# Optimization experiments

Hardware: AMD Instinct MI355X
Metric: run time of the kernel (lower is better)

The kernel has to match this reference:

```python
import jax, jax.numpy as jnp
import numpy as np

B, S, H, D = 4, 2048, 8, 64  # batch, seq, heads, per-head dim (dim=64)
EPS = 1e-5


def _layernorm(h, g, b):
    m = jnp.mean(h, axis=-1, keepdims=True)
    v = jnp.mean(jnp.square(h - m), axis=-1, keepdims=True)
    return (h - m) * jax.lax.rsqrt(v + EPS) * g + b


def setup_inputs() -> dict:
    key = jax.random.key(0)
    ks = jax.random.split(key, 12)
    s = 1.0 / np.sqrt(D)
    return {
        "x": jax.random.normal(ks[0], (B, S, H, D), dtype=jnp.float32),
        "ln1_g": jnp.ones((D,), jnp.float32),
        "ln1_b": jnp.zeros((D,), jnp.float32),
        "Wp": jax.random.normal(ks[1], (D, 3 * D), jnp.float32) * s,
        "bp": jnp.zeros((3 * D,), jnp.float32),
        "ln2_g": jnp.ones((D,), jnp.float32),
        "ln2_b": jnp.zeros((D,), jnp.float32),
        "W1": jax.random.normal(ks[2], (D, 4 * D), jnp.float32) * s,
        "b1": jnp.zeros((4 * D,), jnp.float32),
        "W2": jax.random.normal(ks[3], (4 * D, D), jnp.float32) * (1.0 / np.sqrt(4 * D)),
        "b2": jnp.zeros((D,), jnp.float32),
    }


def reference(x, ln1_g, ln1_b, Wp, bp, ln2_g, ln2_b, W1, b1, W2, b2):
    # x: [B, S, H, D]
    h = _layernorm(x, ln1_g, ln1_b)
    qkv = h @ Wp + bp                       # [B,S,H,3D]  (dropout = identity, eval)
    q, k, v = jnp.split(qkv, 3, axis=-1)
    q = q.transpose(0, 2, 1, 3)             # [B,H,S,D]
    k = k.transpose(0, 2, 1, 3)
    v = v.transpose(0, 2, 1, 3)
    sim = jnp.einsum('bhqd,bhkd->bhqk', q, k)   # no sqrt(d) scaling (faithful)
    attn = jax.nn.softmax(sim, axis=-1)
    out = jnp.einsum('bhqk,bhkd->bhqd', attn, v).transpose(0, 2, 1, 3)  # [B,S,H,D]
    out = _layernorm(out, ln2_g, ln2_b)
    out = jax.nn.gelu(out @ W1 + b1, approximate=False) @ W2 + b2
    return out + x
```

## Files before the change

### kernel.cpp

```cpp
#include <hip/hip_runtime.h>
#include <hip/hip_bf16.h>
#include <math.h>

#define BB 4
#define SS 2048
#define HH 8
#define DD 64
#define EPSV 1e-5f

typedef __attribute__((ext_vector_type(8))) short short8;
typedef __attribute__((ext_vector_type(4))) float f32x4;
typedef __attribute__((ext_vector_type(4))) unsigned int uint4v;
typedef unsigned short ushort_t;
#define MFMA16 __builtin_amdgcn_mfma_f32_16x16x32_bf16

__device__ inline unsigned short f2bf(float f) {
    unsigned u = __builtin_bit_cast(unsigned, f);
    unsigned r = (u + 0x7fffu + ((u >> 16) & 1u)) >> 16;
    return (unsigned short)r;
}
__device__ inline float bf2f(unsigned short h) {
    unsigned u = ((unsigned)h) << 16;
    return __builtin_bit_cast(float, u);
}
__device__ inline unsigned pkbf(float a, float b) {
    __hip_bfloat162 h2 = __float22bfloat162_rn(make_float2(a, b));
    unsigned u;
    __builtin_memcpy(&u, &h2, 4);
    return u;
}

__global__ __launch_bounds__(256) void k0_prep(
    const float* __restrict__ Wp, const float* __restrict__ W1,
    const float* __restrict__ W2, ushort_t* __restrict__ WpTh,
    ushort_t* __restrict__ WpTl, ushort_t* __restrict__ W1T,
    ushort_t* __restrict__ W2T)
{
    int gid = blockIdx.x * 256 + threadIdx.x;
    if (gid < 12288) {
        int n = gid >> 6, k = gid & 63;
        float w = Wp[k * 192 + n];
        ushort_t hi = f2bf(w);
        WpTh[gid] = hi;
        WpTl[gid] = f2bf(w - bf2f(hi));
    }
    {
        int n = gid >> 6, k = gid & 63;
        W1T[gid] = f2bf(W1[k * 256 + n]);
    }
    {
        int n = gid >> 8, k = gid & 255;
        W2T[gid] = f2bf(W2[k * 64 + n]);
    }
}

__global__ __launch_bounds__(256) void k1_ln_qkv(
    const float* __restrict__ x, const float* __restrict__ g1, const float* __restrict__ b1v,
    const ushort_t* __restrict__ WpTh, const ushort_t* __restrict__ WpTl,
    const float* __restrict__ bp,
    float* __restrict__ qws, ushort_t* __restrict__ khws, ushort_t* __restrict__ vtws)
{
    __shared__ __align__(16) ushort_t Hh[64 * 72];
    __shared__ __align__(16) ushort_t Hl[64 * 72];
    __shared__ __align__(16) ushort_t Vt[64 * 72];

    const int tid = threadIdx.x;
    const int wv  = tid >> 6;
    const int lane = tid & 63;
    const int l15 = lane & 15;
    const int g   = lane >> 4;
    const int bh  = blockIdx.x & 31;
    const int sc  = blockIdx.x >> 5;
    const int b   = bh >> 3, hh = bh & 7;
    const int s0  = sc * 64;

    short8 bqh[2], bql[2], bkh[2], bkl[2], bvh[2];
    #pragma unroll
    for (int kh = 0; kh < 2; ++kh) {
        int koff = kh * 32 + g * 8;
        bqh[kh] = *(const short8*)(WpTh + (wv * 16 + l15) * 64 + koff);
        bql[kh] = *(const short8*)(WpTl + (wv * 16 + l15) * 64 + koff);
        bkh[kh] = *(const short8*)(WpTh + (64 + wv * 16 + l15) * 64 + koff);
        bkl[kh] = *(const short8*)(WpTl + (64 + wv * 16 + l15) * 64 + koff);
        bvh[kh] = *(const short8*)(WpTh + (128 + wv * 16 + l15) * 64 + koff);
    }
    const float biasq = bp[wv * 16 + l15];
    const float biask = bp[64 + wv * 16 + l15];
    const float biasv = bp[128 + wv * 16 + l15];

    {
        const int srow = s0 + wv * 16 + l15;
        const float* xr = x + ((size_t)(b * 2048 + srow) * 8 + hh) * 64;
        float hvv[16];
        #pragma unroll
        for (int kh = 0; kh < 2; ++kh) {
            float4 p0 = *(const float4*)(xr + kh * 32 + g * 8);
            float4 p1 = *(const float4*)(xr + kh * 32 + g * 8 + 4);
            hvv[kh*8+0]=p0.x; hvv[kh*8+1]=p0.y; hvv[kh*8+2]=p0.z; hvv[kh*8+3]=p0.w;
            hvv[kh*8+4]=p1.x; hvv[kh*8+5]=p1.y; hvv[kh*8+6]=p1.z; hvv[kh*8+7]=p1.w;
        }
        float s1 = 0.0f;
        #pragma unroll
        for (int i = 0; i < 16; ++i) s1 += hvv[i];
        s1 += __shfl_xor(s1, 16, 64);
        s1 += __shfl_xor(s1, 32, 64);
        float mean = s1 * (1.0f / 64.0f);
        float s2 = 0.0f;
        #pragma unroll
        for (int i = 0; i < 16; ++i) { float d = hvv[i] - mean; s2 += d * d; }
        s2 += __shfl_xor(s2, 16, 64);
        s2 += __shfl_xor(s2, 32, 64);
        float rstd = rsqrtf(s2 * (1.0f / 64.0f) + EPSV);

        #pragma unroll
        for (int kh = 0; kh < 2; ++kh) {
            ushort_t hi[8]; unsigned lo2[4];
            float hf[8];
            #pragma unroll
            for (int j = 0; j < 8; ++j) {
                int dI = kh * 32 + g * 8 + j;
                hf[j] = (hvv[kh*8+j] - mean) * rstd * g1[dI] + b1v[dI];
                hi[j] = f2bf(hf[j]);
            }
            uint4 HHv;
            HHv.x = (unsigned)hi[0] | ((unsigned)hi[1] << 16);
            HHv.y = (unsigned)hi[2] | ((unsigned)hi[3] << 16);
            HHv.z = (unsigned)hi[4] | ((unsigned)hi[5] << 16);
            HHv.w = (unsigned)hi[6] | ((unsigned)hi[7] << 16);
            #pragma unroll
            for (int j = 0; j < 4; ++j)
                lo2[j] = pkbf(hf[2*j] - bf2f(hi[2*j]), hf[2*j+1] - bf2f(hi[2*j+1]));
            uint4 HLv; HLv.x = lo2[0]; HLv.y = lo2[1]; HLv.z = lo2[2]; HLv.w = lo2[3];
            int off = (wv * 16 + l15) * 72 + kh * 32 + g * 8;
            *(uint4*)(&Hh[off]) = HHv;
            *(uint4*)(&Hl[off]) = HLv;
        }
    }
    __syncthreads();

    #pragma unroll
    for (int mt = 0; mt < 4; ++mt) {
        short8 ah[2], al[2];
        int abase = (mt * 16 + l15) * 72 + g * 8;
        ah[0] = *(const short8*)(&Hh[abase]);
        ah[1] = *(const short8*)(&Hh[abase + 32]);
        al[0] = *(const short8*)(&Hl[abase]);
        al[1] = *(const short8*)(&Hl[abase + 32]);

        f32x4 aq = (f32x4){0.f,0.f,0.f,0.f};
        f32x4 ak = (f32x4){0.f,0.f,0.f,0.f};
        f32x4 av = (f32x4){0.f,0.f,0.f,0.f};
        #pragma unroll
        for (int kh = 0; kh < 2; ++kh) {
            aq = MFMA16(ah[kh], bqh[kh], aq, 0, 0, 0);
            aq = MFMA16(al[kh], bqh[kh], aq, 0, 0, 0);
            aq = MFMA16(ah[kh], bql[kh], aq, 0, 0, 0);
            ak = MFMA16(ah[kh], bkh[kh], ak, 0, 0, 0);
            ak = MFMA16(al[kh], bkh[kh], ak, 0, 0, 0);
            ak = MFMA16(ah[kh], bkl[kh], ak, 0, 0, 0);
            av = MFMA16(ah[kh], bvh[kh], av, 0, 0, 0);
        }

        size_t base = ((size_t)bh * 2048 + s0 + mt * 16 + 4 * g) * 64 + wv * 16 + l15;
        #pragma unroll
        for (int r = 0; r < 4; ++r) {
            qws[base + (size_t)r * 64] = aq[r] + biasq;
            khws[base + (size_t)r * 64] = f2bf(ak[r] + biask);
        }
        uint2 vvp;
        vvp.x = pkbf(av[0] + biasv, av[1] + biasv);
        vvp.y = pkbf(av[2] + biasv, av[3] + biasv);
        *(uint2*)(&Vt[(wv * 16 + l15) * 72 + mt * 16 + 4 * g]) = vvp;
    }
    __syncthreads();

    #pragma unroll
    for (int p = 0; p < 2; ++p) {
        int slot = tid + 256 * p;
        int dd = slot >> 3, cc = slot & 7;
        int c0 = ((cc >> 2) << 5) + ((cc & 3) << 2);
        uint2 a = *(const uint2*)(&Vt[dd * 72 + c0]);
        uint2 b2 = *(const uint2*)(&Vt[dd * 72 + c0 + 16]);
        uint4 o; o.x = a.x; o.y = a.y; o.z = b2.x; o.w = b2.y;
        *(uint4*)(vtws + ((size_t)bh * 64 + dd) * 2048 + s0 + cc * 8) = o;
    }
}

#define LROW 72
#define NKT 32

__global__ __launch_bounds__(256, 4) void k2_attn(
    const float* __restrict__ qws, const ushort_t* __restrict__ khws,
    const ushort_t* __restrict__ vtws, float* __restrict__ ows)
{
    __shared__ __align__(16) ushort_t KhL[2][64 * LROW];
    __shared__ __align__(16) ushort_t VtL[2][64 * LROW];

    const int tid  = threadIdx.x;
    const int w    = tid >> 6;
    const int lane = tid & 63;
    const int l15  = lane & 15;
    const int g    = lane >> 4;
    const int bh   = blockIdx.x & 31;
    const int qb0  = (blockIdx.x >> 5) * 128;

    const float LOG2E = 1.4426950408889634f;
    short8 qh[2][2], ql[2][2];
    #pragma unroll
    for (int sub = 0; sub < 2; ++sub) {
        const float* qp = qws + ((size_t)bh * SS + qb0 + w * 32 + sub * 16 + l15) * 64;
        #pragma unroll
        for (int kh = 0; kh < 2; ++kh) {
            const float* p = qp + 32 * kh + 8 * g;
            #pragma unroll
            for (int j = 0; j < 8; ++j) {
                float f = p[j] * LOG2E;
                ushort_t hi = f2bf(f);
                qh[sub][kh][j] = (short)hi;
                ql[sub][kh][j] = (short)f2bf(f - bf2f(hi));
            }
        }
    }

    float lrow[2] = {0.0f, 0.0f};
    f32x4 oacc[2][4];
    #pragma unroll
    for (int sub = 0; sub < 2; ++sub)
        #pragma unroll
        for (int dt = 0; dt < 4; ++dt) oacc[sub][dt] = (f32x4){0.f, 0.f, 0.f, 0.f};

    const size_t kbase = (size_t)bh * SS * 64;
    const size_t vbase = (size_t)bh * 64 * 2048;

    uint4 kb[2], vb[2];
    #pragma unroll
    for (int rr = 0; rr < 2; ++rr) {
        int slot = tid + 256 * rr;
        int row = slot >> 3, seg = slot & 7;
        kb[rr] = *(const uint4*)(khws + kbase + (size_t)row * 64 + seg * 8);
        vb[rr] = *(const uint4*)(vtws + vbase + (size_t)row * 2048 + seg * 8);
    }
    #pragma unroll
    for (int rr = 0; rr < 2; ++rr) {
        int slot = tid + 256 * rr;
        int row = slot >> 3, seg = slot & 7;
        *(uint4*)(&KhL[0][row * LROW + seg * 8]) = kb[rr];
        *(uint4*)(&VtL[0][row * LROW + seg * 8]) = vb[rr];
    }

    for (int kt = 0; kt < NKT; ++kt) {
        __syncthreads();
        const int cur = kt & 1;

        if (kt < NKT - 1) {
            #pragma unroll
            for (int rr = 0; rr < 2; ++rr) {
                int slot = tid + 256 * rr;
                int row = slot >> 3, seg = slot & 7;
                kb[rr] = *(const uint4*)(khws + kbase + (size_t)((kt + 1) * 64 + row) * 64 + seg * 8);
                vb[rr] = *(const uint4*)(vtws + vbase + (size_t)row * 2048 + (kt + 1) * 64 + seg * 8);
            }
        }

        #pragma unroll
        for (int half = 0; half < 2; ++half) {
            uint2 pA[2], pB[2];
            #pragma unroll
            for (int nf2 = 0; nf2 < 2; ++nf2) {
                const int nf = half * 2 + nf2;
                f32x4 aA = (f32x4){0.f, 0.f, 0.f, 0.f};
                f32x4 aB = (f32x4){0.f, 0.f, 0.f, 0.f};
                #pragma unroll
                for (int kh = 0; kh < 2; ++kh) {
                    short8 kah = *(const short8*)(&KhL[cur][(nf * 16 + l15) * LROW + 32 * kh + 8 * g]);
                    aA = MFMA16(kah, qh[0][kh], aA, 0, 0, 0);
                    aA = MFMA16(kah, ql[0][kh], aA, 0, 0, 0);
                    aB = MFMA16(kah, qh[1][kh], aB, 0, 0, 0);
                    aB = MFMA16(kah, ql[1][kh], aB, 0, 0, 0);
                }
                {
                    float p0 = __builtin_amdgcn_exp2f(aA[0]);
                    float p1 = __builtin_amdgcn_exp2f(aA[1]);
                    float p2 = __builtin_amdgcn_exp2f(aA[2]);
                    float p3 = __builtin_amdgcn_exp2f(aA[3]);
                    lrow[0] += (p0 + p1) + (p2 + p3);
                    pA[nf2].x = pkbf(p0, p1); pA[nf2].y = pkbf(p2, p3);
                }
                {
                    float p0 = __builtin_amdgcn_exp2f(aB[0]);
                    float p1 = __builtin_amdgcn_exp2f(aB[1]);
                    float p2 = __builtin_amdgcn_exp2f(aB[2]);
                    float p3 = __builtin_amdgcn_exp2f(aB[3]);
                    lrow[1] += (p0 + p1) + (p2 + p3);
                    pB[nf2].x = pkbf(p0, p1); pB[nf2].y = pkbf(p2, p3);
                }
            }
            short8 paA = __builtin_bit_cast(short8, (uint4v){pA[0].x, pA[0].y, pA[1].x, pA[1].y});
            short8 paB = __builtin_bit_cast(short8, (uint4v){pB[0].x, pB[0].y, pB[1].x, pB[1].y});
            #pragma unroll
            for (int dt = 0; dt < 4; ++dt) {
                short8 vbf = *(const short8*)(&VtL[cur][(16 * dt + l15) * LROW + half * 32 + 8 * g]);
                oacc[0][dt] = MFMA16(paA, vbf, oacc[0][dt], 0, 0, 0);
                oacc[1][dt] = MFMA16(paB, vbf, oacc[1][dt], 0, 0, 0);
            }
        }

        if (kt < NKT - 1) {
            #pragma unroll
            for (int rr = 0; rr < 2; ++rr) {
                int slot = tid + 256 * rr;
                int row = slot >> 3, seg = slot & 7;
                *(uint4*)(&KhL[cur ^ 1][row * LROW + seg * 8]) = kb[rr];
                *(uint4*)(&VtL[cur ^ 1][row * LROW + seg * 8]) = vb[rr];
            }
        }
    }

    #pragma unroll
    for (int sub = 0; sub < 2; ++sub) {
        float l = lrow[sub];
        l += __shfl_xor(l, 16, 64);
        l += __shfl_xor(l, 32, 64);
        float il = 1.0f / l;
        #pragma unroll
        for (int r = 0; r < 4; ++r) {
            float ilr = __shfl(il, 4 * g + r, 64);
            int row = qb0 + w * 32 + sub * 16 + 4 * g + r;
            #pragma unroll
            for (int dt = 0; dt < 4; ++dt)
                ows[((size_t)bh * SS + row) * 64 + dt * 16 + l15] = oacc[sub][dt][r] * ilr;
        }
    }
}

#define ITERS 4

__global__ __launch_bounds__(256) void k3_ln_mlp(
    const float* __restrict__ ows, const float* __restrict__ x,
    const float* __restrict__ g2, const float* __restrict__ b2v,
    const ushort_t* __restrict__ W1T, const float* __restrict__ b1m,
    const ushort_t* __restrict__ W2T, const float* __restrict__ b2o,
    float* __restrict__ out)
{
    __shared__ __align__(16) ushort_t Hs[16 * 264];
    __shared__ __align__(16) float Rs[4 * 16 * 72];

    const int tid  = threadIdx.x;
    const int wv   = tid >> 6;
    const int lane = tid & 63;
    const int l15  = lane & 15;
    const int g    = lane >> 4;

    short8 w1f[4][2], w2f[4][2];
    float  b1r[4][4];
    #pragma unroll
    for (int t = 0; t < 4; ++t) {
        #pragma unroll
        for (int kh = 0; kh < 2; ++kh) {
            w1f[t][kh] = *(const short8*)(W1T + (wv * 64 + t * 16 + l15) * 64 + kh * 32 + g * 8);
            w2f[t][kh] = *(const short8*)(W2T + (t * 16 + l15) * 256 + wv * 64 + kh * 32 + g * 8);
        }
        #pragma unroll
        for (int r = 0; r < 4; ++r)
            b1r[t][r] = b1m[wv * 64 + t * 16 + 4 * g + r];
    }

    for (int it = 0; it < ITERS; ++it) {
        const int r0 = (blockIdx.x * ITERS + it) * 16;

        const float* orow = ows + (size_t)(r0 + l15) * 64;
        float hvv[16];
        #pragma unroll
        for (int kh = 0; kh < 2; ++kh) {
            float4 p0 = *(const float4*)(orow + kh * 32 + g * 8);
            float4 p1 = *(const float4*)(orow + kh * 32 + g * 8 + 4);
            hvv[kh*8+0]=p0.x; hvv[kh*8+1]=p0.y; hvv[kh*8+2]=p0.z; hvv[kh*8+3]=p0.w;
            hvv[kh*8+4]=p1.x; hvv[kh*8+5]=p1.y; hvv[kh*8+6]=p1.z; hvv[kh*8+7]=p1.w;
        }
        float s1 = 0.0f;
        #pragma unroll
        for (int i = 0; i < 16; ++i) s1 += hvv[i];
        s1 += __shfl_xor(s1, 16, 64);
        s1 += __shfl_xor(s1, 32, 64);
        float mean = s1 * (1.0f / 64.0f);
        float s2 = 0.0f;
        #pragma unroll
        for (int i = 0; i < 16; ++i) { float d = hvv[i] - mean; s2 += d * d; }
        s2 += __shfl_xor(s2, 16, 64);
        s2 += __shfl_xor(s2, 32, 64);
        float rstd = rsqrtf(s2 * (1.0f / 64.0f) + EPSV);

        short8 h2f[2];
        #pragma unroll
        for (int kh = 0; kh < 2; ++kh) {
            float4 ga = *(const float4*)(g2 + kh * 32 + g * 8);
            float4 gb = *(const float4*)(g2 + kh * 32 + g * 8 + 4);
            float4 ba = *(const float4*)(b2v + kh * 32 + g * 8);
            float4 bb = *(const float4*)(b2v + kh * 32 + g * 8 + 4);
            float gg[8] = {ga.x,ga.y,ga.z,ga.w,gb.x,gb.y,gb.z,gb.w};
            float bv[8] = {ba.x,ba.y,ba.z,ba.w,bb.x,bb.y,bb.z,bb.w};
            #pragma unroll
            for (int j = 0; j < 8; ++j)
                h2f[kh][j] = (short)f2bf((hvv[kh*8+j] - mean) * rstd * gg[j] + bv[j]);
        }

        #pragma unroll
        for (int t = 0; t < 4; ++t) {
            f32x4 acc = (f32x4){0.f, 0.f, 0.f, 0.f};
            acc = MFMA16(w1f[t][0], h2f[0], acc, 0, 0, 0);
            acc = MFMA16(w1f[t][1], h2f[1], acc, 0, 0, 0);
            float ge[4];
            #pragma unroll
            for (int r = 0; r < 4; ++r) {
                float v = acc[r] + b1r[t][r];
                ge[r] = 0.5f * v * (1.0f + erff(v * 0.70710678118654752f));
            }
            uint2 pk;
            pk.x = pkbf(ge[0], ge[1]);
            pk.y = pkbf(ge[2], ge[3]);
            *(uint2*)(&Hs[l15 * 264 + wv * 64 + t * 16 + 4 * g]) = pk;
        }

        short8 ha[2];
        ha[0] = *(const short8*)(&Hs[l15 * 264 + wv * 64 + g * 8]);
        ha[1] = *(const short8*)(&Hs[l15 * 264 + wv * 64 + 32 + g * 8]);
        #pragma unroll
        for (int t = 0; t < 4; ++t) {
            f32x4 a2 = (f32x4){0.f, 0.f, 0.f, 0.f};
            a2 = MFMA16(ha[0], w2f[t][0], a2, 0, 0, 0);
            a2 = MFMA16(ha[1], w2f[t][1], a2, 0, 0, 0);
            #pragma unroll
            for (int r = 0; r < 4; ++r)
                Rs[wv * 1152 + (4 * g + r) * 72 + t * 16 + l15] = a2[r];
        }
        __syncthreads();

        {
            int m = tid >> 4, d4 = tid & 15;
            const float* rp = Rs + m * 72 + d4 * 4;
            f32x4 v0 = *(const f32x4*)(rp);
            f32x4 v1 = *(const f32x4*)(rp + 1152);
            f32x4 v2 = *(const f32x4*)(rp + 2304);
            f32x4 v3 = *(const f32x4*)(rp + 3456);
            f32x4 sum = v0 + v1 + v2 + v3;
            int r = r0 + m;
            int bq = r >> 14, hq = (r >> 11) & 7, sq = r & 2047;
            size_t oidx = ((size_t)(bq * 2048 + sq) * 8 + hq) * 64 + d4 * 4;
            float4 xv = *(const float4*)(x + oidx);
            float4 bo = *(const float4*)(b2o + d4 * 4);
            float4 res = make_float4(sum[0] + xv.x + bo.x, sum[1] + xv.y + bo.y,
                                     sum[2] + xv.z + bo.z, sum[3] + xv.w + bo.w);
            *(float4*)(out + oidx) = res;
        }
        __syncthreads();
    }
}

extern "C" void kernel_launch(void* const* d_in, const int* in_sizes, int n_in,
                              void* d_out, int out_size, void* d_ws, size_t ws_size,
                              hipStream_t stream) {
    const float* x     = (const float*)d_in[0];
    const float* ln1_g = (const float*)d_in[1];
    const float* ln1_b = (const float*)d_in[2];
    const float* Wp    = (const float*)d_in[3];
    const float* bp    = (const float*)d_in[4];
    const float* ln2_g = (const float*)d_in[5];
    const float* ln2_b = (const float*)d_in[6];
    const float* W1    = (const float*)d_in[7];
    const float* b1    = (const float*)d_in[8];
    const float* W2    = (const float*)d_in[9];
    const float* b2    = (const float*)d_in[10];
    float* out = (float*)d_out;

    float* ws  = (float*)d_ws;
    float* qws = ws;
    float* ows = ws + 4194304;
    ushort_t* khws = (ushort_t*)(ws + 8388608);
    ushort_t* vtws = khws + 4194304;
    ushort_t* WpTh = vtws + 4194304;
    ushort_t* WpTl = WpTh + 12288;
    ushort_t* W1T  = WpTl + 12288;
    ushort_t* W2T  = W1T + 16384;

    k0_prep<<<dim3(64), dim3(256), 0, stream>>>(Wp, W1, W2, WpTh, WpTl, W1T, W2T);
    k1_ln_qkv<<<dim3(1024), dim3(256), 0, stream>>>(
        x, ln1_g, ln1_b, WpTh, WpTl, bp, qws, khws, vtws);
    k2_attn<<<dim3(512), dim3(256), 0, stream>>>(qws, khws, vtws, ows);
    k3_ln_mlp<<<dim3(BB * HH * SS / 16 / ITERS), dim3(256), 0, stream>>>(
        ows, x, ln2_g, ln2_b, W1T, b1, W2T, b2, out);
}
```

Baseline: 204.9 us.

## Split attention key range across two wave groups per block and combine

The attention kernel now launches 512 threads per block, with two groups of four waves each covering half of the key sequence for the same 128 queries. Partial outputs and row sums from the second group are combined through shared memory at the end. Because there is no running max, the two partial results can simply be added. This doubles wave-level parallelism over the 512 blocks to improve latency hiding, since 512 blocks of 4 waves underfill the GPU. In exchange, the double-buffered LDS ping-pong becomes a single buffer with an extra barrier per tile, and a shared-memory reduction is added at the end.

```diff
diff --git a/kernel.cpp b/kernel.cpp
--- a/kernel.cpp
+++ b/kernel.cpp
@@ -187,20 +187,22 @@
 }
 
 #define LROW 72
-#define NKT 32
-
-__global__ __launch_bounds__(256, 4) void k2_attn(
+#define NKTH 16
+
+__global__ __launch_bounds__(512, 2) void k2_attn(
     const float* __restrict__ qws, const ushort_t* __restrict__ khws,
     const ushort_t* __restrict__ vtws, float* __restrict__ ows)
 {
-    __shared__ __align__(16) ushort_t KhL[2][64 * LROW];
-    __shared__ __align__(16) ushort_t VtL[2][64 * LROW];
+    __shared__ __align__(16) ushort_t SM[2][2][64 * LROW];
 
     const int tid  = threadIdx.x;
     const int w    = tid >> 6;
+    const int hw   = w >> 2;
+    const int w4   = w & 3;
     const int lane = tid & 63;
     const int l15  = lane & 15;
     const int g    = lane >> 4;
+    const int tid4 = tid & 255;
     const int bh   = blockIdx.x & 31;
     const int qb0  = (blockIdx.x >> 5) * 128;
 
@@ -208,7 +210,7 @@
     short8 qh[2][2], ql[2][2];
     #pragma unroll
     for (int sub = 0; sub < 2; ++sub) {
-        const float* qp = qws + ((size_t)bh * SS + qb0 + w * 32 + sub * 16 + l15) * 64;
+        const float* qp = qws + ((size_t)bh * SS + qb0 + w4 * 32 + sub * 16 + l15) * 64;
         #pragma unroll
         for (int kh = 0; kh < 2; ++kh) {
             const float* p = qp + 32 * kh + 8 * g;
@@ -232,34 +234,34 @@
     const size_t kbase = (size_t)bh * SS * 64;
     const size_t vbase = (size_t)bh * 64 * 2048;
 
+    const int row0 = (tid4) >> 3,        seg0 = tid4 & 7;
+    const int row1 = (tid4 + 256) >> 3,  seg1 = (tid4 + 256) & 7;
+
     uint4 kb[2], vb[2];
-    #pragma unroll
-    for (int rr = 0; rr < 2; ++rr) {
-        int slot = tid + 256 * rr;
-        int row = slot >> 3, seg = slot & 7;
-        kb[rr] = *(const uint4*)(khws + kbase + (size_t)row * 64 + seg * 8);
-        vb[rr] = *(const uint4*)(vtws + vbase + (size_t)row * 2048 + seg * 8);
-    }
-    #pragma unroll
-    for (int rr = 0; rr < 2; ++rr) {
-        int slot = tid + 256 * rr;
-        int row = slot >> 3, seg = slot & 7;
-        *(uint4*)(&KhL[0][row * LROW + seg * 8]) = kb[rr];
-        *(uint4*)(&VtL[0][row * LROW + seg * 8]) = vb[rr];
-    }
-
-    for (int kt = 0; kt < NKT; ++kt) {
+    {
+        int tg = hw * NKTH;
+        kb[0] = *(const uint4*)(khws + kbase + (size_t)(tg * 64 + row0) * 64 + seg0 * 8);
+        vb[0] = *(const uint4*)(vtws + vbase + (size_t)row0 * 2048 + tg * 64 + seg0 * 8);
+        kb[1] = *(const uint4*)(khws + kbase + (size_t)(tg * 64 + row1) * 64 + seg1 * 8);
+        vb[1] = *(const uint4*)(vtws + vbase + (size_t)row1 * 2048 + tg * 64 + seg1 * 8);
+    }
+
+    for (int kt = 0; kt < NKTH; ++kt) {
         __syncthreads();
-        const int cur = kt & 1;
-
-        if (kt < NKT - 1) {
-            #pragma unroll
-            for (int rr = 0; rr < 2; ++rr) {
-                int slot = tid + 256 * rr;
-                int row = slot >> 3, seg = slot & 7;
-                kb[rr] = *(const uint4*)(khws + kbase + (size_t)((kt + 1) * 64 + row) * 64 + seg * 8);
-                vb[rr] = *(const uint4*)(vtws + vbase + (size_t)row * 2048 + (kt + 1) * 64 + seg * 8);
-            }
+        *(uint4*)(&SM[hw][0][row0 * LROW + seg0 * 8]) = kb[0];
+        *(uint4*)(&SM[hw][1][row0 * LROW + seg0 * 8]) = vb[0];
+        *(uint4*)(&SM[hw][0][row1 * LROW + seg1 * 8]) = kb[1];
+        *(uint4*)(&SM[hw][1][row1 * LROW + seg1 * 8]) = vb[1];
+        __syncthreads();
+        const ushort_t* KhL = &SM[hw][0][0];
+        const ushort_t* VtL = &SM[hw][1][0];
+
+        if (kt < NKTH - 1) {
+            int tg = hw * NKTH + kt + 1;
+            kb[0] = *(const uint4*)(khws + kbase + (size_t)(tg * 64 + row0) * 64 + seg0 * 8);
+            vb[0] = *(const uint4*)(vtws + vbase + (size_t)row0 * 2048 + tg * 64 + seg0 * 8);
+            kb[1] = *(const uint4*)(khws + kbase + (size_t)(tg * 64 + row1) * 64 + seg1 * 8);
+            vb[1] = *(const uint4*)(vtws + vbase + (size_t)row1 * 2048 + tg * 64 + seg1 * 8);
         }
 
         #pragma unroll
@@ -272,7 +274,7 @@
                 f32x4 aB = (f32x4){0.f, 0.f, 0.f, 0.f};
                 #pragma unroll
                 for (int kh = 0; kh < 2; ++kh) {
-                    short8 kah = *(const short8*)(&KhL[cur][(nf * 16 + l15) * LROW + 32 * kh + 8 * g]);
+                    short8 kah = *(const short8*)(&KhL[(nf * 16 + l15) * LROW + 32 * kh + 8 * g]);
                     aA = MFMA16(kah, qh[0][kh], aA, 0, 0, 0);
                     aA = MFMA16(kah, ql[0][kh], aA, 0, 0, 0);
                     aB = MFMA16(kah, qh[1][kh], aB, 0, 0, 0);
@@ -299,21 +301,34 @@
             short8 paB = __builtin_bit_cast(short8, (uint4v){pB[0].x, pB[0].y, pB[1].x, pB[1].y});
             #pragma unroll
             for (int dt = 0; dt < 4; ++dt) {
-                short8 vbf = *(const short8*)(&VtL[cur][(16 * dt + l15) * LROW + half * 32 + 8 * g]);
+                short8 vbf = *(const short8*)(&VtL[(16 * dt + l15) * LROW + half * 32 + 8 * g]);
                 oacc[0][dt] = MFMA16(paA, vbf, oacc[0][dt], 0, 0, 0);
                 oacc[1][dt] = MFMA16(paB, vbf, oacc[1][dt], 0, 0, 0);
             }
         }
-
-        if (kt < NKT - 1) {
-            #pragma unroll
-            for (int rr = 0; rr < 2; ++rr) {
-                int slot = tid + 256 * rr;
-                int row = slot >> 3, seg = slot & 7;
-                *(uint4*)(&KhL[cur ^ 1][row * LROW + seg * 8]) = kb[rr];
-                *(uint4*)(&VtL[cur ^ 1][row * LROW + seg * 8]) = vb[rr];
-            }
-        }
+    }
+
+    __syncthreads();
+    float* cmb = (float*)&SM[0][0][0];
+    float* rec = cmb + (w4 * 64 + lane) * 36;
+    if (hw == 1) {
+        #pragma unroll
+        for (int sub = 0; sub < 2; ++sub) {
+            #pragma unroll
+            for (int dt = 0; dt < 4; ++dt)
+                *(f32x4*)(rec + sub * 16 + dt * 4) = oacc[sub][dt];
+            rec[32 + sub] = lrow[sub];
+        }
+    }
+    __syncthreads();
+    if (hw == 1) return;
+
+    #pragma unroll
+    for (int sub = 0; sub < 2; ++sub) {
+        #pragma unroll
+        for (int dt = 0; dt < 4; ++dt)
+            oacc[sub][dt] += *(const f32x4*)(rec + sub * 16 + dt * 4);
+        lrow[sub] += rec[32 + sub];
     }
 
     #pragma unroll
@@ -325,7 +340,7 @@
         #pragma unroll
         for (int r = 0; r < 4; ++r) {
             float ilr = __shfl(il, 4 * g + r, 64);
-            int row = qb0 + w * 32 + sub * 16 + 4 * g + r;
+            int row = qb0 + w4 * 32 + sub * 16 + 4 * g + r;
             #pragma unroll
             for (int dt = 0; dt < 4; ++dt)
                 ows[((size_t)bh * SS + row) * 64 + dt * 16 + l15] = oacc[sub][dt][r] * ilr;
@@ -485,7 +500,7 @@
     k0_prep<<<dim3(64), dim3(256), 0, stream>>>(Wp, W1, W2, WpTh, WpTl, W1T, W2T);
     k1_ln_qkv<<<dim3(1024), dim3(256), 0, stream>>>(
         x, ln1_g, ln1_b, WpTh, WpTl, bp, qws, khws, vtws);
-    k2_attn<<<dim3(512), dim3(256), 0, stream>>>(qws, khws, vtws, ows);
+    k2_attn<<<dim3(512), dim3(512), 0, stream>>>(qws, khws, vtws, ows);
     k3_ln_mlp<<<dim3(BB * HH * SS / 16 / ITERS), dim3(256), 0, stream>>>(
         ows, x, ln2_g, ln2_b, W1T, b1, W2T, b2, out);
 }
```

New measurement: 243.7 us. +18.9%, slower.
